# Kernel tuning notes

Hardware: AMD Instinct MI355X
Metric: run time of the kernel (lower is better)

## Reference

```python
import jax, jax.numpy as jnp
import numpy as np
from functools import lru_cache

SEG_GROUPS = 2          # len(segment_lengths) = len([1024, 2048])
HEAD_DIM = 64
SCALE = HEAD_DIM ** -0.5


@lru_cache(maxsize=None)
def _hilbert_perm(n: int):
    """Replicates _generate_hilbert_indices. For n a perfect power of 4 this is a
    true permutation (and its inverse)."""
    dim = 1
    while dim * dim < n:
        dim *= 2
    idxs = []
    for i in range(min(n, dim * dim)):
        x = y = 0
        s = 1
        t = i
        while s < dim:
            rx = 1 & (t // 2)
            ry = 1 & (t ^ rx)
            if ry == 0:
                if rx == 1:
                    x, y = dim and (s - 1 - y), (s - 1 - x)
                x, y = y, x
            x += s * rx
            y += s * ry
            t //= 4
            s *= 2
        cell = x * dim + y
        if cell < n:
            idxs.append(cell)
    if len(idxs) < n:
        idxs.extend(range(len(idxs), n))
    hil = np.asarray(idxs[:n], dtype=np.int64)
    inv = np.zeros(n, dtype=np.int64)
    inv[hil] = np.arange(n, dtype=np.int64)
    return hil, inv


def setup_inputs() -> dict:
    key = jax.random.key(0)
    k1, k2, k3 = jax.random.split(key, 3)
    shape = (4, 4096, 16, 64)  # [batch, seq_len, num_heads, head_dim]
    return {
        "q": jax.random.normal(k1, shape, dtype=jnp.float32),
        "k": jax.random.normal(k2, shape, dtype=jnp.float32),
        "v": jax.random.normal(k3, shape, dtype=jnp.float32),
    }


def reference(q, k, v):
    """Faithful translation of RingDilatedAttentionHilbertOptimizedFixed.forward
    with is_causal=False, dropout=0, dilation_rates=[1,1].

    Fidelity notes:
    - The torch code matmuls [B, L, h, d] @ [B, L, d, h] WITHOUT moving heads to a
      batch dim, so scores are [B, L, h, h]: per-position head-vs-head attention.
      With dilation_rate=1 this makes the segment loop a pure partition of the
      sequence, so we vectorize over the whole (Hilbert-ordered) sequence.
    - Hilbert gather on q/k/v and inverse scatter on the output are kept.
    """
    B, S, H, D = q.shape
    hil_np, inv_np = _hilbert_perm(S)
    hil = jnp.asarray(hil_np)
    inv = jnp.asarray(inv_np)

    # Hilbert-curve reordering along the sequence axis.
    qo = jnp.take(q, hil, axis=1)
    ko = jnp.take(k, hil, axis=1)
    vo = jnp.take(v, hil, axis=1)

    hg = max(1, H // SEG_GROUPS)  # heads_per_segment
    outs = []
    for g in range(SEG_GROUPS):
        hs, he = g * hg, min(g * hg + hg, H)
        qs, ks, vs = qo[:, :, hs:he], ko[:, :, hs:he], vo[:, :, hs:he]
        # per-position head-vs-head scores: [B, S, hg, hg]
        scores = jnp.einsum("bsid,bsjd->bsij", qs, ks) * SCALE
        attn = jax.nn.softmax(scores, axis=-1)
        attn = jnp.nan_to_num(attn, nan=0.0)
        outs.append(jnp.einsum("bsij,bsjd->bsid", attn, vs))
    out = jnp.concatenate(outs, axis=2)  # heads fully covered: 2 * 8 = 16

    # Inverse Hilbert reordering.
    return jnp.take(out, inv, axis=1)
```

## Files before the change

kernel.cpp:

```cpp
#include <hip/hip_runtime.h>
#include <math.h>


#define HEADS 16
#define DIM 64
#define GH 8
#define GFLOATS (GH * DIM)
#define WSLICE (2 * GFLOATS)
#define WPB 4

typedef float f32x4 __attribute__((ext_vector_type(4)));

__global__ void __launch_bounds__(256, 8) hilbert_attn_kernel(
    const float* __restrict__ q,
    const float* __restrict__ k,
    const float* __restrict__ v,
    float* __restrict__ out,
    int npos)
{
    __shared__ float lds[WPB * WSLICE];
    const int wave = threadIdx.x >> 6;
    const int lane = threadIdx.x & 63;

    const long long w   = (long long)blockIdx.x * WPB + wave;
    const long long pos = w >> 1;
    const int       grp = (int)(w & 1);
    if (pos >= npos) return;

    float* kk = lds + wave * WSLICE;
    float* vv = kk + GFLOATS;

    const long long gbase = pos * (HEADS * DIM) + (long long)grp * GFLOATS;

    const int i = lane >> 3;
    const int s = lane & 7;

    const float* qp = q + gbase + i * DIM + s * 8;
    f32x4 q0 = *(const f32x4*)(qp + 0);
    f32x4 q1 = *(const f32x4*)(qp + 4);

#pragma unroll
    for (int r = 0; r < 2; ++r) {
        const int fo = r * 256 + lane * 4;
        f32x4 a = *(const f32x4*)(k + gbase + fo);
        f32x4 b = *(const f32x4*)(v + gbase + fo);
        *(f32x4*)(kk + fo) = a;
        *(f32x4*)(vv + fo) = b;
    }

    float sc[8];
#pragma unroll
    for (int j = 0; j < 8; ++j) {
        const float* kr = kk + j * DIM + s * 8;
        f32x4 p = q0 * *(const f32x4*)(kr + 0)
                + q1 * *(const f32x4*)(kr + 4);
        sc[j] = p.x + p.y + p.z + p.w;
    }
#pragma unroll
    for (int j = 0; j < 8; ++j) {
        sc[j] += __shfl_xor(sc[j], 1);
        sc[j] += __shfl_xor(sc[j], 2);
        sc[j] += __shfl_xor(sc[j], 4);
        sc[j] *= 0.125f;
    }

    float m = sc[0];
#pragma unroll
    for (int j = 1; j < 8; ++j) m = fmaxf(m, sc[j]);
    float at[8];
    float sum = 0.f;
#pragma unroll
    for (int j = 0; j < 8; ++j) { at[j] = __expf(sc[j] - m); sum += at[j]; }
    const float inv = 1.f / sum;
#pragma unroll
    for (int j = 0; j < 8; ++j) at[j] *= inv;

    f32x4 o0 = {0.f, 0.f, 0.f, 0.f};
    f32x4 o1 = o0;
#pragma unroll
    for (int j = 0; j < 8; ++j) {
        const float a = at[j];
        const float* vr = vv + j * DIM + s * 8;
        o0 += a * *(const f32x4*)(vr + 0);
        o1 += a * *(const f32x4*)(vr + 4);
    }

    float* op = out + gbase + i * DIM + s * 8;
    *(f32x4*)(op + 0) = o0;
    *(f32x4*)(op + 4) = o1;
}

extern "C" void kernel_launch(void* const* d_in, const int* in_sizes, int n_in,
                              void* d_out, int out_size, void* d_ws, size_t ws_size,
                              hipStream_t stream) {
    const float* q = (const float*)d_in[0];
    const float* k = (const float*)d_in[1];
    const float* v = (const float*)d_in[2];
    float* out = (float*)d_out;

    const int npos = in_sizes[0] / (HEADS * DIM);
    const long long nwaves = 2LL * npos;
    const int blocks = (int)((nwaves + WPB - 1) / WPB);
    hilbert_attn_kernel<<<blocks, WPB * 64, 0, stream>>>(q, k, v, out, npos);
}
```

Measured before the change: 211.6 us.

## Double-buffer K/V via direct global-to-LDS loads in a persistent grid-stride loop

```diff
diff --git a/kernel.cpp b/kernel.cpp
--- a/kernel.cpp
+++ b/kernel.cpp
@@ -6,100 +6,155 @@
 #define DIM 64
 #define GH 8
 #define GFLOATS (GH * DIM)
-#define WSLICE (2 * GFLOATS)
+#define BUFF (2 * GFLOATS)
+#define WSLICE (2 * BUFF)
 #define WPB 4
 
 typedef float f32x4 __attribute__((ext_vector_type(4)));
 
-__global__ void __launch_bounds__(256, 8) hilbert_attn_kernel(
+#define GLD16(gsrc, ldst_base) \
+  __builtin_amdgcn_global_load_lds( \
+      (const __attribute__((address_space(1))) unsigned int*)(gsrc), \
+      (__attribute__((address_space(3))) unsigned int*)(ldst_base), 16, 0, 0)
+
+template <int N>
+__device__ __forceinline__ void wait_vmcnt() {
+  asm volatile("s_waitcnt vmcnt(%0)" ::"n"(N) : "memory");
+  __builtin_amdgcn_sched_barrier(0);
+}
+
+__device__ __forceinline__ void stage(const float* __restrict__ q,
+                                      const float* __restrict__ k,
+                                      const float* __restrict__ v,
+                                      long long gbase, int lane,
+                                      float* buf, f32x4& q0, f32x4& q1) {
+  GLD16(k + gbase + lane * 4,       buf);
+  GLD16(k + gbase + 256 + lane * 4, buf + 256);
+  GLD16(v + gbase + lane * 4,       buf + 512);
+  GLD16(v + gbase + 256 + lane * 4, buf + 768);
+  const int i = lane >> 3, s = lane & 7;
+  const float* qp = q + gbase + i * DIM + s * 8;
+  q0 = *(const f32x4*)(qp + 0);
+  q1 = *(const f32x4*)(qp + 4);
+}
+
+__device__ __forceinline__ void compute(const float* buf, int lane,
+                                        f32x4 q0, f32x4 q1,
+                                        f32x4& o0, f32x4& o1) {
+  const int s = lane & 7;
+  const float* kk = buf;
+  const float* vv = buf + GFLOATS;
+
+  float sc[8];
+#pragma unroll
+  for (int j = 0; j < 8; ++j) {
+    const float* kr = kk + j * DIM + s * 8;
+    f32x4 p = q0 * *(const f32x4*)(kr + 0) + q1 * *(const f32x4*)(kr + 4);
+    sc[j] = p.x + p.y + p.z + p.w;
+  }
+#pragma unroll
+  for (int j = 0; j < 8; ++j) {
+    sc[j] += __shfl_xor(sc[j], 1);
+    sc[j] += __shfl_xor(sc[j], 2);
+    sc[j] += __shfl_xor(sc[j], 4);
+    sc[j] *= 0.125f;
+  }
+  float m = sc[0];
+#pragma unroll
+  for (int j = 1; j < 8; ++j) m = fmaxf(m, sc[j]);
+  float at[8];
+  float sum = 0.f;
+#pragma unroll
+  for (int j = 0; j < 8; ++j) { at[j] = __expf(sc[j] - m); sum += at[j]; }
+  const float inv = 1.f / sum;
+
+  o0 = (f32x4){0.f, 0.f, 0.f, 0.f};
+  o1 = o0;
+#pragma unroll
+  for (int j = 0; j < 8; ++j) {
+    const float a = at[j] * inv;
+    const float* vr = vv + j * DIM + s * 8;
+    o0 += a * *(const f32x4*)(vr + 0);
+    o1 += a * *(const f32x4*)(vr + 4);
+  }
+}
+
+__device__ __forceinline__ long long task_base(long long t) {
+  return (t >> 1) * (long long)(HEADS * DIM) + (t & 1) * (long long)GFLOATS;
+}
+
+__global__ void __launch_bounds__(256, 5) hilbert_attn_kernel(
     const float* __restrict__ q,
     const float* __restrict__ k,
     const float* __restrict__ v,
     float* __restrict__ out,
     int npos)
 {
-    __shared__ float lds[WPB * WSLICE];
-    const int wave = threadIdx.x >> 6;
-    const int lane = threadIdx.x & 63;
+  __shared__ float lds[WPB * WSLICE];
+  const int wave = threadIdx.x >> 6;
+  const int lane = threadIdx.x & 63;
+  const long long S  = (long long)gridDim.x * WPB;
+  const long long NT = 2LL * npos;
 
-    const long long w   = (long long)blockIdx.x * WPB + wave;
-    const long long pos = w >> 1;
-    const int       grp = (int)(w & 1);
-    if (pos >= npos) return;
+  long long t = (long long)blockIdx.x * WPB + wave;
+  if (t >= NT) return;
 
-    float* kk = lds + wave * WSLICE;
-    float* vv = kk + GFLOATS;
+  float* buf0 = lds + wave * WSLICE;
+  float* buf1 = buf0 + BUFF;
+  const int i = lane >> 3, s = lane & 7;
+  const long long lofs = (long long)(i * DIM + s * 8);
 
-    const long long gbase = pos * (HEADS * DIM) + (long long)grp * GFLOATS;
+  f32x4 qA0, qA1, qB0, qB1, o0, o1;
 
-    const int i = lane >> 3;
-    const int s = lane & 7;
+  stage(q, k, v, task_base(t), lane, buf0, qA0, qA1);
+  if (t + S < NT) {
+    stage(q, k, v, task_base(t + S), lane, buf1, qB0, qB1);
+    wait_vmcnt<6>();
+  } else {
+    wait_vmcnt<0>();
+  }
 
-    const float* qp = q + gbase + i * DIM + s * 8;
-    f32x4 q0 = *(const f32x4*)(qp + 0);
-    f32x4 q1 = *(const f32x4*)(qp + 4);
-
-#pragma unroll
-    for (int r = 0; r < 2; ++r) {
-        const int fo = r * 256 + lane * 4;
-        f32x4 a = *(const f32x4*)(k + gbase + fo);
-        f32x4 b = *(const f32x4*)(v + gbase + fo);
-        *(f32x4*)(kk + fo) = a;
-        *(f32x4*)(vv + fo) = b;
+  for (;;) {
+    compute(buf0, lane, qA0, qA1, o0, o1);
+    {
+      asm volatile("s_waitcnt lgkmcnt(0)" ::: "memory");
+      __builtin_amdgcn_sched_barrier(0);
+      const bool pf = (t + 2 * S < NT);
+      if (pf) stage(q, k, v, task_base(t + 2 * S), lane, buf0, qA0, qA1);
+      float* op = out + task_base(t) + lofs;
+      *(f32x4*)(op + 0) = o0;
+      *(f32x4*)(op + 4) = o1;
+      t += S;
+      if (t >= NT) return;
+      if (pf) wait_vmcnt<8>(); else wait_vmcnt<2>();
     }
-
-    float sc[8];
-#pragma unroll
-    for (int j = 0; j < 8; ++j) {
-        const float* kr = kk + j * DIM + s * 8;
-        f32x4 p = q0 * *(const f32x4*)(kr + 0)
-                + q1 * *(const f32x4*)(kr + 4);
-        sc[j] = p.x + p.y + p.z + p.w;
+    compute(buf1, lane, qB0, qB1, o0, o1);
+    {
+      asm volatile("s_waitcnt lgkmcnt(0)" ::: "memory");
+      __builtin_amdgcn_sched_barrier(0);
+      const bool pf = (t + 2 * S < NT);
+      if (pf) stage(q, k, v, task_base(t + 2 * S), lane, buf1, qB0, qB1);
+      float* op = out + task_base(t) + lofs;
+      *(f32x4*)(op + 0) = o0;
+      *(f32x4*)(op + 4) = o1;
+      t += S;
+      if (t >= NT) return;
+      if (pf) wait_vmcnt<8>(); else wait_vmcnt<2>();
     }
-#pragma unroll
-    for (int j = 0; j < 8; ++j) {
-        sc[j] += __shfl_xor(sc[j], 1);
-        sc[j] += __shfl_xor(sc[j], 2);
-        sc[j] += __shfl_xor(sc[j], 4);
-        sc[j] *= 0.125f;
-    }
-
-    float m = sc[0];
-#pragma unroll
-    for (int j = 1; j < 8; ++j) m = fmaxf(m, sc[j]);
-    float at[8];
-    float sum = 0.f;
-#pragma unroll
-    for (int j = 0; j < 8; ++j) { at[j] = __expf(sc[j] - m); sum += at[j]; }
-    const float inv = 1.f / sum;
-#pragma unroll
-    for (int j = 0; j < 8; ++j) at[j] *= inv;
-
-    f32x4 o0 = {0.f, 0.f, 0.f, 0.f};
-    f32x4 o1 = o0;
-#pragma unroll
-    for (int j = 0; j < 8; ++j) {
-        const float a = at[j];
-        const float* vr = vv + j * DIM + s * 8;
-        o0 += a * *(const f32x4*)(vr + 0);
-        o1 += a * *(const f32x4*)(vr + 4);
-    }
-
-    float* op = out + gbase + i * DIM + s * 8;
-    *(f32x4*)(op + 0) = o0;
-    *(f32x4*)(op + 4) = o1;
+  }
 }
 
 extern "C" void kernel_launch(void* const* d_in, const int* in_sizes, int n_in,
                               void* d_out, int out_size, void* d_ws, size_t ws_size,
                               hipStream_t stream) {
-    const float* q = (const float*)d_in[0];
-    const float* k = (const float*)d_in[1];
-    const float* v = (const float*)d_in[2];
-    float* out = (float*)d_out;
+  const float* q = (const float*)d_in[0];
+  const float* k = (const float*)d_in[1];
+  const float* v = (const float*)d_in[2];
+  float* out = (float*)d_out;
 
-    const int npos = in_sizes[0] / (HEADS * DIM);
-    const long long nwaves = 2LL * npos;
-    const int blocks = (int)((nwaves + WPB - 1) / WPB);
-    hilbert_attn_kernel<<<blocks, WPB * 64, 0, stream>>>(q, k, v, out, npos);
+  const int npos = in_sizes[0] / (HEADS * DIM);
+  const long long ntasks = 2LL * npos;
+  const long long nwaves = (ntasks + 3) / 4;
+  const int blocks = (int)((nwaves + WPB - 1) / WPB);
+  hilbert_attn_kernel<<<blocks, WPB * 64, 0, stream>>>(q, k, v, out, npos);
 }
```

Measured after the change: 242.1 us. 1.14x slower.
